# Optimization experiments

Measured on AMD Instinct MI355X. Metric: run time of the kernel, lower is better.

Reference implementation:

```python
import jax, jax.numpy as jnp
import numpy as np

B, S, D_IN, D_OUT, E = 4, 2048, 1024, 1024, 8

def setup_inputs() -> dict:
    key = jax.random.key(0)
    ks = jax.random.split(key, 5)
    scale = 1.0 / np.sqrt(D_IN)
    x  = jax.random.normal(ks[0], (B, S, D_IN), dtype=jnp.float32)
    We = jax.random.uniform(ks[1], (E, D_OUT, D_IN), dtype=jnp.float32, minval=-scale, maxval=scale)
    be = jax.random.uniform(ks[2], (E, D_OUT), dtype=jnp.float32, minval=-scale, maxval=scale)
    Wg = jax.random.uniform(ks[3], (E, D_IN), dtype=jnp.float32, minval=-scale, maxval=scale)
    bg = jax.random.uniform(ks[4], (E,), dtype=jnp.float32, minval=-scale, maxval=scale)
    return {"x": x, "We": We, "be": be, "Wg": Wg, "bg": bg}

def reference(x, We, be, Wg, bg):
    # gate: [B,S,E]
    gate_logits = jnp.einsum('bsd,ed->bse', x, Wg) + bg
    gate = jax.nn.softmax(gate_logits, axis=-1)
    top1 = jnp.argmax(gate, axis=-1)                      # [B,S]
    one_hot = jax.nn.one_hot(top1, E, dtype=x.dtype)      # [B,S,E]
    # all-expert dense outputs, stacked on last axis: [B,S,O,E]
    expert_outs = jnp.einsum('bsd,eod->bsoe', x, We) + be.T
    out = jnp.einsum('bsoe,bse->bso', expert_outs, one_hot)
    mean_gate = gate.mean(axis=(0, 1))                    # [E]
    aux_loss = jnp.mean((mean_gate * E) ** 2)
    return (out, aux_loss)
```

## Files before the change

kernel.cpp:

```cpp
#include <hip/hip_runtime.h>
#include <hip/hip_bf16.h>


#define NTOK 8192
#define DIN  1024
#define DOUT 1024
#define NE   8

typedef unsigned short u16;
typedef unsigned int   u32;
typedef unsigned long long u64;
typedef short  bf16x8 __attribute__((ext_vector_type(8)));
typedef float  f32x4  __attribute__((ext_vector_type(4)));

__device__ __forceinline__ u16 f2bf(float f) {
    __hip_bfloat16 h = __float2bfloat16(f);
    return *(u16*)&h;
}


__global__ __launch_bounds__(256) void gate_kernel(
    const float* __restrict__ x, const float* __restrict__ Wg,
    const float* __restrict__ bg, u32* __restrict__ stage)
{
    __shared__ int   am_s[16];
    __shared__ float mg_s[4][NE];

    const int tid  = threadIdx.x;
    const int wave = tid >> 6;
    const int lane = tid & 63;
    const int g    = lane >> 3;
    const int sub  = lane & 7;

    const float* wr = Wg + g * DIN + 4 * sub;

    float bgl[NE];
    #pragma unroll
    for (int e = 0; e < NE; ++e) bgl[e] = bg[e];

    float mgacc = 0.f;

    #pragma unroll 1
    for (int it = 0; it < 4; ++it) {
        const int t = blockIdx.x * 16 + wave * 4 + it;
        const float* xr = x + (size_t)t * DIN + 4 * sub;

        float acc0 = 0.f, acc1 = 0.f, acc2 = 0.f, acc3 = 0.f;
        #pragma unroll
        for (int j = 0; j < 8; ++j) {
            const int k = j * 128;
            f32x4 x0 = *(const f32x4*)(xr + k);
            f32x4 w0 = *(const f32x4*)(wr + k);
            f32x4 x1 = *(const f32x4*)(xr + k + 32);
            f32x4 w1 = *(const f32x4*)(wr + k + 32);
            f32x4 x2 = *(const f32x4*)(xr + k + 64);
            f32x4 w2 = *(const f32x4*)(wr + k + 64);
            f32x4 x3 = *(const f32x4*)(xr + k + 96);
            f32x4 w3 = *(const f32x4*)(wr + k + 96);
            #pragma unroll
            for (int q = 0; q < 4; ++q) {
                acc0 = fmaf(w0[q], x0[q], acc0);
                acc1 = fmaf(w1[q], x1[q], acc1);
                acc2 = fmaf(w2[q], x2[q], acc2);
                acc3 = fmaf(w3[q], x3[q], acc3);
            }
        }
        float acc = (acc0 + acc1) + (acc2 + acc3);

        acc += __shfl_xor(acc, 1, 64);
        acc += __shfl_xor(acc, 2, 64);
        acc += __shfl_xor(acc, 4, 64);

        float logit[NE];
        #pragma unroll
        for (int e = 0; e < NE; ++e)
            logit[e] = __shfl(acc, e * 8, 64) + bgl[e];

        float m = logit[0]; int am = 0;
        #pragma unroll
        for (int e = 1; e < NE; ++e) if (logit[e] > m) { m = logit[e]; am = e; }

        float p[NE], s = 0.f;
        #pragma unroll
        for (int e = 0; e < NE; ++e) { p[e] = __expf(logit[e] - m); s += p[e]; }
        const float inv = 1.f / s;

        float psel = p[0];
        #pragma unroll
        for (int e = 1; e < NE; ++e) psel = (lane == e) ? p[e] : psel;
        if (lane < NE) mgacc += psel * inv;

        if (lane == 0) am_s[wave * 4 + it] = am;
    }

    if (lane < NE) mg_s[wave][lane] = mgacc;
    __syncthreads();

    u32* rec = stage + (size_t)blockIdx.x * 16;
    if (tid == 0) {
        u64 pack = 0;
        #pragma unroll
        for (int i = 0; i < 16; ++i) pack |= (u64)am_s[i] << (4 * i);
        *(u64*)rec = pack;
    }
    if (tid < NE) {
        float s = mg_s[0][tid] + mg_s[1][tid] + mg_s[2][tid] + mg_s[3][tid];
        rec[2 + tid] = __float_as_uint(s);
    }
}

__global__ __launch_bounds__(512) void route_kernel(
    const u32* __restrict__ stage, int* __restrict__ counts,
    int* __restrict__ tok_list, float* __restrict__ out)
{
    __shared__ float mgl[512][NE];
    __shared__ int   c[512][9];
    __shared__ float tot_s[NE];

    const int tid  = threadIdx.x;
    const int wave = tid >> 6;
    const int lane = tid & 63;

    const u64 pack = *(const u64*)(stage + (size_t)tid * 16);
    #pragma unroll
    for (int e = 0; e < NE; ++e)
        mgl[tid][e] = __uint_as_float(stage[tid * 16 + 2 + e]);

    #pragma unroll
    for (int e = 0; e < 9; ++e) c[tid][e] = 0;

    #pragma unroll
    for (int it = 0; it < 16; ++it) {
        int e3 = (int)((pack >> (4 * it)) & 7);
        c[tid][e3]++;
    }
    __syncthreads();

    {
        const int e = wave;
        int carry = 0;
        #pragma unroll 1
        for (int ch = 0; ch < 8; ++ch) {
            int v = c[ch * 64 + lane][e];
            int incl = v;
            #pragma unroll
            for (int off = 1; off < 64; off <<= 1) {
                int n = __shfl_up(incl, off, 64);
                if (lane >= off) incl += n;
            }
            c[ch * 64 + lane][e] = incl - v + carry;
            carry += __shfl(incl, 63, 64);
        }
        if (lane == 0) counts[e] = carry;
    }
    __syncthreads();

    #pragma unroll
    for (int it = 0; it < 16; ++it) {
        int e3 = (int)((pack >> (4 * it)) & 7);
        int pos = c[tid][e3]++;
        tok_list[e3 * NTOK + pos] = tid * 16 + it;
    }

    {
        const int e = wave;
        float s = 0.f;
        #pragma unroll
        for (int ch = 0; ch < 8; ++ch) s += mgl[ch * 64 + lane][e];
        #pragma unroll
        for (int off = 32; off > 0; off >>= 1) s += __shfl_xor(s, off, 64);
        if (lane == 0) tot_s[e] = s;
    }
    __syncthreads();
    if (tid == 0) {
        float s = 0.f;
        #pragma unroll
        for (int e = 0; e < NE; ++e) {
            float m = tot_s[e] * (8.0f / 8192.0f);
            s += m * m;
        }
        out[(size_t)NTOK * DOUT] = s * 0.125f;
    }
}

__global__ __launch_bounds__(256) void moe_gemm(
    const float* __restrict__ x, const float* __restrict__ We,
    const float* __restrict__ be, const int* __restrict__ counts,
    const int* __restrict__ tok_list, float* __restrict__ out)
{
    const int e   = blockIdx.z;
    const int cnt = counts[e];
    const int m0  = blockIdx.y * 64;
    if (m0 >= cnt) return;
    const int n0  = blockIdx.x * 128;

    __shared__ u16 sA[64 * 64];
    __shared__ u16 sB[128 * 64];
    __shared__ int toks[64];

    const int tid = threadIdx.x;
    if (tid < 64) {
        int gr = m0 + tid;
        toks[tid] = (gr < cnt) ? tok_list[e * NTOK + gr] : tok_list[e * NTOK];
    }
    __syncthreads();

    const int lane = tid & 63;
    const int wave = tid >> 6;
    const int wn   = wave * 32;
    const int lrow = lane & 15;
    const int quad = lane >> 4;
    const int l7   = lrow & 7;

    f32x4 acc[4][2];
    #pragma unroll
    for (int i = 0; i < 4; ++i)
        #pragma unroll
        for (int j = 0; j < 2; ++j) acc[i][j] = (f32x4){0.f, 0.f, 0.f, 0.f};

    const int srow = tid >> 3;
    const int ch   = tid & 7;
    const int cx   = ch ^ (srow & 7);

    const float* aS[2];
    const float* bS[4];
    #pragma unroll
    for (int s = 0; s < 2; ++s)
        aS[s] = x + (size_t)toks[srow + 32 * s] * DIN + ch * 8;
    #pragma unroll
    for (int s = 0; s < 4; ++s)
        bS[s] = We + ((size_t)e << 20) + ((size_t)(n0 + srow + 32 * s) << 10) + ch * 8;

    f32x4 ar[2][2], br[4][2];

    #define LOADR(k0)                                            \
        do {                                                     \
            _Pragma("unroll")                                    \
            for (int s = 0; s < 2; ++s) {                        \
                ar[s][0] = *(const f32x4*)(aS[s] + (k0));        \
                ar[s][1] = *(const f32x4*)(aS[s] + (k0) + 4);    \
            }                                                    \
            _Pragma("unroll")                                    \
            for (int s = 0; s < 4; ++s) {                        \
                br[s][0] = *(const f32x4*)(bS[s] + (k0));        \
                br[s][1] = *(const f32x4*)(bS[s] + (k0) + 4);    \
            }                                                    \
        } while (0)

    #define STOREW()                                                     \
        do {                                                             \
            _Pragma("unroll")                                            \
            for (int s = 0; s < 2; ++s) {                                \
                union { u16 h[8]; uint4 u; } ua;                         \
                _Pragma("unroll")                                        \
                for (int q = 0; q < 4; ++q) {                            \
                    ua.h[q]     = f2bf(ar[s][0][q]);                     \
                    ua.h[4 + q] = f2bf(ar[s][1][q]);                     \
                }                                                        \
                *(uint4*)&sA[(srow + 32 * s) * 64 + cx * 8] = ua.u;      \
            }                                                            \
            _Pragma("unroll")                                            \
            for (int s = 0; s < 4; ++s) {                                \
                union { u16 h[8]; uint4 u; } ub;                         \
                _Pragma("unroll")                                        \
                for (int q = 0; q < 4; ++q) {                            \
                    ub.h[q]     = f2bf(br[s][0][q]);                     \
                    ub.h[4 + q] = f2bf(br[s][1][q]);                     \
                }                                                        \
                *(uint4*)&sB[(srow + 32 * s) * 64 + cx * 8] = ub.u;      \
            }                                                            \
        } while (0)

    #define COMPUTE()                                                         \
        do {                                                                  \
            bf16x8 af[2][4], bv[2][2];                                        \
            _Pragma("unroll")                                                 \
            for (int ks = 0; ks < 2; ++ks) {                                  \
                const int so = ((ks * 4 + quad) ^ l7) * 8;                    \
                _Pragma("unroll")                                             \
                for (int i = 0; i < 4; ++i)                                   \
                    af[ks][i] = *(const bf16x8*)&sA[(i * 16 + lrow) * 64 + so]; \
                _Pragma("unroll")                                             \
                for (int j = 0; j < 2; ++j)                                   \
                    bv[ks][j] = *(const bf16x8*)&sB[(wn + j * 16 + lrow) * 64 + so]; \
            }                                                                 \
            _Pragma("unroll")                                                 \
            for (int ks = 0; ks < 2; ++ks)                                    \
                _Pragma("unroll")                                             \
                for (int i = 0; i < 4; ++i)                                   \
                    _Pragma("unroll")                                         \
                    for (int j = 0; j < 2; ++j)                               \
                        acc[i][j] = __builtin_amdgcn_mfma_f32_16x16x32_bf16(  \
                            af[ks][i], bv[ks][j], acc[i][j], 0, 0, 0);        \
        } while (0)

    LOADR(0);
    #pragma unroll 1
    for (int k0 = 0; k0 < DIN; k0 += 64) {
        __syncthreads();
        STOREW();
        if (k0 + 64 < DIN) LOADR(k0 + 64);
        __syncthreads();
        COMPUTE();
    }

    #undef LOADR
    #undef STOREW
    #undef COMPUTE

    #pragma unroll
    for (int j = 0; j < 2; ++j) {
        const int col = n0 + wn + j * 16 + lrow;
        const float bev = be[e * DOUT + col];
        #pragma unroll
        for (int i = 0; i < 4; ++i) {
            #pragma unroll
            for (int r = 0; r < 4; ++r) {
                const int rl = i * 16 + quad * 4 + r;
                if (m0 + rl < cnt) {
                    const int tok = toks[rl];
                    out[((size_t)tok << 10) + col] = acc[i][j][r] + bev;
                }
            }
        }
    }
}

extern "C" void kernel_launch(void* const* d_in, const int* in_sizes, int n_in,
                              void* d_out, int out_size, void* d_ws, size_t ws_size,
                              hipStream_t stream) {
    const float* x  = (const float*)d_in[0];
    const float* We = (const float*)d_in[1];
    const float* be = (const float*)d_in[2];
    const float* Wg = (const float*)d_in[3];
    const float* bg = (const float*)d_in[4];
    float* out = (float*)d_out;

    int* counts   = (int*)d_ws;
    int* tok_list = (int*)((char*)d_ws + 256);
    u32* stage    = (u32*)((char*)d_ws + 256);

    gate_kernel<<<512, 256, 0, stream>>>(x, Wg, bg, stage);
    route_kernel<<<1, 512, 0, stream>>>(stage, counts, tok_list, out);
    moe_gemm<<<dim3(8, 128, 8), 256, 0, stream>>>(x, We, be, counts, tok_list, out);
}
```

Baseline: 182.0 us.

## Fuse gate and routing kernels using a last-block-done atomic pattern

Merges the gate kernel and the single-block route kernel into one launch. Each block bumps an atomic completion counter, and the last block to finish does the expert counting, prefix scan, token list build and aux loss. The gate loop is also restructured so the Wg slice is loaded once and reused across the four tokens a wave handles, which gives more independent loads in flight. In exchange, a hipMemsetAsync is added to reset the counter, and the routing tail now runs on a 256-thread block that handles two records per thread.

Result: slower. 248.9 us (+36.8%).

```diff
diff --git a/kernel.cpp b/kernel.cpp
--- a/kernel.cpp
+++ b/kernel.cpp
@@ -19,167 +19,198 @@
 }
 
 
-__global__ __launch_bounds__(256) void gate_kernel(
+__global__ __launch_bounds__(256) void gate_route_kernel(
     const float* __restrict__ x, const float* __restrict__ Wg,
-    const float* __restrict__ bg, u32* __restrict__ stage)
+    const float* __restrict__ bg, int* __restrict__ counts,
+    int* __restrict__ done, int* __restrict__ tok_list,
+    u32* __restrict__ stage, float* __restrict__ out)
 {
-    __shared__ int   am_s[16];
-    __shared__ float mg_s[4][NE];
+    __shared__ union {
+        struct { int am[16]; float mg[4][NE]; } gt;
+        struct { int cnt[512][9]; float mgred[4][NE]; } r;
+    } sm;
+    __shared__ int isLast;
 
     const int tid  = threadIdx.x;
+    const int bid  = blockIdx.x;
     const int wave = tid >> 6;
     const int lane = tid & 63;
     const int g    = lane >> 3;
     const int sub  = lane & 7;
 
-    const float* wr = Wg + g * DIN + 4 * sub;
-
-    float bgl[NE];
-    #pragma unroll
-    for (int e = 0; e < NE; ++e) bgl[e] = bg[e];
-
-    float mgacc = 0.f;
-
-    #pragma unroll 1
-    for (int it = 0; it < 4; ++it) {
-        const int t = blockIdx.x * 16 + wave * 4 + it;
-        const float* xr = x + (size_t)t * DIN + 4 * sub;
-
-        float acc0 = 0.f, acc1 = 0.f, acc2 = 0.f, acc3 = 0.f;
+    {
+        const float* wr = Wg + g * DIN + 4 * sub;
+        const float* xr[4];
+        #pragma unroll
+        for (int it = 0; it < 4; ++it)
+            xr[it] = x + (size_t)(bid * 16 + wave * 4 + it) * DIN + 4 * sub;
+
+        float acc[4][4];
+        #pragma unroll
+        for (int it = 0; it < 4; ++it)
+            #pragma unroll
+            for (int c = 0; c < 4; ++c) acc[it][c] = 0.f;
+
         #pragma unroll
         for (int j = 0; j < 8; ++j) {
             const int k = j * 128;
-            f32x4 x0 = *(const f32x4*)(xr + k);
             f32x4 w0 = *(const f32x4*)(wr + k);
-            f32x4 x1 = *(const f32x4*)(xr + k + 32);
             f32x4 w1 = *(const f32x4*)(wr + k + 32);
-            f32x4 x2 = *(const f32x4*)(xr + k + 64);
             f32x4 w2 = *(const f32x4*)(wr + k + 64);
-            f32x4 x3 = *(const f32x4*)(xr + k + 96);
             f32x4 w3 = *(const f32x4*)(wr + k + 96);
             #pragma unroll
-            for (int q = 0; q < 4; ++q) {
-                acc0 = fmaf(w0[q], x0[q], acc0);
-                acc1 = fmaf(w1[q], x1[q], acc1);
-                acc2 = fmaf(w2[q], x2[q], acc2);
-                acc3 = fmaf(w3[q], x3[q], acc3);
-            }
-        }
-        float acc = (acc0 + acc1) + (acc2 + acc3);
-
-        acc += __shfl_xor(acc, 1, 64);
-        acc += __shfl_xor(acc, 2, 64);
-        acc += __shfl_xor(acc, 4, 64);
-
-        float logit[NE];
-        #pragma unroll
-        for (int e = 0; e < NE; ++e)
-            logit[e] = __shfl(acc, e * 8, 64) + bgl[e];
-
-        float m = logit[0]; int am = 0;
-        #pragma unroll
-        for (int e = 1; e < NE; ++e) if (logit[e] > m) { m = logit[e]; am = e; }
-
-        float p[NE], s = 0.f;
-        #pragma unroll
-        for (int e = 0; e < NE; ++e) { p[e] = __expf(logit[e] - m); s += p[e]; }
-        const float inv = 1.f / s;
-
-        float psel = p[0];
-        #pragma unroll
-        for (int e = 1; e < NE; ++e) psel = (lane == e) ? p[e] : psel;
-        if (lane < NE) mgacc += psel * inv;
-
-        if (lane == 0) am_s[wave * 4 + it] = am;
-    }
-
-    if (lane < NE) mg_s[wave][lane] = mgacc;
-    __syncthreads();
-
-    u32* rec = stage + (size_t)blockIdx.x * 16;
-    if (tid == 0) {
-        u64 pack = 0;
-        #pragma unroll
-        for (int i = 0; i < 16; ++i) pack |= (u64)am_s[i] << (4 * i);
-        *(u64*)rec = pack;
-    }
-    if (tid < NE) {
-        float s = mg_s[0][tid] + mg_s[1][tid] + mg_s[2][tid] + mg_s[3][tid];
-        rec[2 + tid] = __float_as_uint(s);
-    }
-}
-
-__global__ __launch_bounds__(512) void route_kernel(
-    const u32* __restrict__ stage, int* __restrict__ counts,
-    int* __restrict__ tok_list, float* __restrict__ out)
-{
-    __shared__ float mgl[512][NE];
-    __shared__ int   c[512][9];
-    __shared__ float tot_s[NE];
-
-    const int tid  = threadIdx.x;
-    const int wave = tid >> 6;
-    const int lane = tid & 63;
-
-    const u64 pack = *(const u64*)(stage + (size_t)tid * 16);
-    #pragma unroll
-    for (int e = 0; e < NE; ++e)
-        mgl[tid][e] = __uint_as_float(stage[tid * 16 + 2 + e]);
-
-    #pragma unroll
-    for (int e = 0; e < 9; ++e) c[tid][e] = 0;
-
-    #pragma unroll
-    for (int it = 0; it < 16; ++it) {
-        int e3 = (int)((pack >> (4 * it)) & 7);
-        c[tid][e3]++;
-    }
-    __syncthreads();
-
-    {
-        const int e = wave;
-        int carry = 0;
-        #pragma unroll 1
-        for (int ch = 0; ch < 8; ++ch) {
-            int v = c[ch * 64 + lane][e];
-            int incl = v;
-            #pragma unroll
-            for (int off = 1; off < 64; off <<= 1) {
-                int n = __shfl_up(incl, off, 64);
-                if (lane >= off) incl += n;
-            }
-            c[ch * 64 + lane][e] = incl - v + carry;
-            carry += __shfl(incl, 63, 64);
-        }
-        if (lane == 0) counts[e] = carry;
-    }
-    __syncthreads();
-
-    #pragma unroll
-    for (int it = 0; it < 16; ++it) {
-        int e3 = (int)((pack >> (4 * it)) & 7);
-        int pos = c[tid][e3]++;
-        tok_list[e3 * NTOK + pos] = tid * 16 + it;
-    }
-
-    {
-        const int e = wave;
-        float s = 0.f;
-        #pragma unroll
-        for (int ch = 0; ch < 8; ++ch) s += mgl[ch * 64 + lane][e];
-        #pragma unroll
-        for (int off = 32; off > 0; off >>= 1) s += __shfl_xor(s, off, 64);
-        if (lane == 0) tot_s[e] = s;
-    }
+            for (int it = 0; it < 4; ++it) {
+                f32x4 x0 = *(const f32x4*)(xr[it] + k);
+                f32x4 x1 = *(const f32x4*)(xr[it] + k + 32);
+                f32x4 x2 = *(const f32x4*)(xr[it] + k + 64);
+                f32x4 x3 = *(const f32x4*)(xr[it] + k + 96);
+                #pragma unroll
+                for (int q = 0; q < 4; ++q) {
+                    acc[it][0] = fmaf(w0[q], x0[q], acc[it][0]);
+                    acc[it][1] = fmaf(w1[q], x1[q], acc[it][1]);
+                    acc[it][2] = fmaf(w2[q], x2[q], acc[it][2]);
+                    acc[it][3] = fmaf(w3[q], x3[q], acc[it][3]);
+                }
+            }
+        }
+
+        float bgl[NE];
+        #pragma unroll
+        for (int e = 0; e < NE; ++e) bgl[e] = bg[e];
+
+        float mgacc = 0.f;
+        #pragma unroll
+        for (int it = 0; it < 4; ++it) {
+            float a = (acc[it][0] + acc[it][1]) + (acc[it][2] + acc[it][3]);
+            a += __shfl_xor(a, 1, 64);
+            a += __shfl_xor(a, 2, 64);
+            a += __shfl_xor(a, 4, 64);
+
+            float logit[NE];
+            #pragma unroll
+            for (int e = 0; e < NE; ++e)
+                logit[e] = __shfl(a, e * 8, 64) + bgl[e];
+
+            float m = logit[0]; int am = 0;
+            #pragma unroll
+            for (int e = 1; e < NE; ++e) if (logit[e] > m) { m = logit[e]; am = e; }
+
+            float p[NE], s = 0.f;
+            #pragma unroll
+            for (int e = 0; e < NE; ++e) { p[e] = __expf(logit[e] - m); s += p[e]; }
+            const float inv = 1.f / s;
+
+            float psel = p[0];
+            #pragma unroll
+            for (int e = 1; e < NE; ++e) psel = (lane == e) ? p[e] : psel;
+            if (lane < NE) mgacc += psel * inv;
+
+            if (lane == 0) sm.gt.am[wave * 4 + it] = am;
+        }
+
+        if (lane < NE) sm.gt.mg[wave][lane] = mgacc;
+        __syncthreads();
+
+        u32* rec = stage + (size_t)bid * 16;
+        if (tid == 0) {
+            u64 pack = 0;
+            #pragma unroll
+            for (int i = 0; i < 16; ++i) pack |= (u64)sm.gt.am[i] << (4 * i);
+            *(u64*)rec = pack;
+        }
+        if (tid < NE) {
+            float s = sm.gt.mg[0][tid] + sm.gt.mg[1][tid]
+                    + sm.gt.mg[2][tid] + sm.gt.mg[3][tid];
+            rec[2 + tid] = __float_as_uint(s);
+        }
+    }
+
+    __threadfence();
     __syncthreads();
     if (tid == 0) {
-        float s = 0.f;
-        #pragma unroll
-        for (int e = 0; e < NE; ++e) {
-            float m = tot_s[e] * (8.0f / 8192.0f);
-            s += m * m;
-        }
-        out[(size_t)NTOK * DOUT] = s * 0.125f;
+        int old = __hip_atomic_fetch_add(done, 1, __ATOMIC_ACQ_REL,
+                                         __HIP_MEMORY_SCOPE_AGENT);
+        isLast = (old == 511);
+    }
+    __syncthreads();
+    if (!isLast) return;
+    __threadfence();
+
+    {
+        u64 pk[2];
+        float mgr[NE];
+        #pragma unroll
+        for (int e = 0; e < NE; ++e) mgr[e] = 0.f;
+        #pragma unroll
+        for (int r = 0; r < 2; ++r) {
+            const u32* rec = stage + (size_t)(2 * tid + r) * 16;
+            pk[r] = *(const u64*)rec;
+            #pragma unroll
+            for (int e = 0; e < NE; ++e) mgr[e] += __uint_as_float(rec[2 + e]);
+        }
+        __syncthreads();
+        #pragma unroll
+        for (int r = 0; r < 2; ++r) {
+            int c8[NE];
+            #pragma unroll
+            for (int e = 0; e < NE; ++e) c8[e] = 0;
+            #pragma unroll
+            for (int it = 0; it < 16; ++it) c8[(int)((pk[r] >> (4 * it)) & 7)]++;
+            #pragma unroll
+            for (int e = 0; e < NE; ++e) sm.r.cnt[2 * tid + r][e] = c8[e];
+        }
+        __syncthreads();
+
+        #pragma unroll
+        for (int half = 0; half < 2; ++half) {
+            const int e = wave + 4 * half;
+            int carry = 0;
+            #pragma unroll 1
+            for (int chn = 0; chn < 8; ++chn) {
+                int v = sm.r.cnt[chn * 64 + lane][e];
+                int incl = v;
+                #pragma unroll
+                for (int off = 1; off < 64; off <<= 1) {
+                    int nn = __shfl_up(incl, off, 64);
+                    if (lane >= off) incl += nn;
+                }
+                sm.r.cnt[chn * 64 + lane][e] = incl - v + carry;
+                carry += __shfl(incl, 63, 64);
+            }
+            if (lane == 0) counts[e] = carry;
+        }
+        __syncthreads();
+
+        #pragma unroll
+        for (int r = 0; r < 2; ++r) {
+            const int rec = 2 * tid + r;
+            #pragma unroll
+            for (int it = 0; it < 16; ++it) {
+                int e3 = (int)((pk[r] >> (4 * it)) & 7);
+                int pos = sm.r.cnt[rec][e3]++;
+                tok_list[e3 * NTOK + pos] = rec * 16 + it;
+            }
+        }
+
+        #pragma unroll
+        for (int e = 0; e < NE; ++e)
+            #pragma unroll
+            for (int off = 32; off > 0; off >>= 1)
+                mgr[e] += __shfl_xor(mgr[e], off, 64);
+        if (lane == 0)
+            #pragma unroll
+            for (int e = 0; e < NE; ++e) sm.r.mgred[wave][e] = mgr[e];
+        __syncthreads();
+        if (tid == 0) {
+            float s = 0.f;
+            #pragma unroll
+            for (int e = 0; e < NE; ++e) {
+                float m = (sm.r.mgred[0][e] + sm.r.mgred[1][e]
+                         + sm.r.mgred[2][e] + sm.r.mgred[3][e]) * (8.0f / 8192.0f);
+                s += m * m;
+            }
+            out[(size_t)NTOK * DOUT] = s * 0.125f;
+        }
     }
 }
 
@@ -337,10 +368,12 @@
     float* out = (float*)d_out;
 
     int* counts   = (int*)d_ws;
+    int* done     = (int*)((char*)d_ws + 32);
     int* tok_list = (int*)((char*)d_ws + 256);
     u32* stage    = (u32*)((char*)d_ws + 256);
 
-    gate_kernel<<<512, 256, 0, stream>>>(x, Wg, bg, stage);
-    route_kernel<<<1, 512, 0, stream>>>(stage, counts, tok_list, out);
+    hipMemsetAsync(d_ws, 0, 64, stream);
+    gate_route_kernel<<<512, 256, 0, stream>>>(x, Wg, bg, counts, done,
+                                               tok_list, stage, out);
     moe_gemm<<<dim3(8, 128, 8), 256, 0, stream>>>(x, We, be, counts, tok_list, out);
 }
```
